# Performance work log

Hardware: AMD Instinct MI355X
Metric: run time of the kernel (lower is better)

## Reference

```python
import jax, jax.numpy as jnp
import numpy as np


def setup_inputs() -> dict:
    key = jax.random.key(0)
    ks = jax.random.split(key, 8)
    B, N, D, H = 8, 512, 64, 64
    user_embeddings = jax.random.normal(ks[0], (B, N, D), dtype=jnp.float32)
    past_lengths = jax.random.randint(ks[1], (B,), 0, N)
    valid_mask = jnp.ones((B, N), dtype=jnp.float32)
    # MLP params: Linear(4D -> H), PReLU (single slope), Linear(H -> 1)
    s1 = 1.0 / np.sqrt(4 * D)
    s2 = 1.0 / np.sqrt(H)
    W1 = jax.random.uniform(ks[2], (H, 4 * D), minval=-s1, maxval=s1, dtype=jnp.float32)
    b1 = jax.random.uniform(ks[3], (H,), minval=-s1, maxval=s1, dtype=jnp.float32)
    prelu_a = jnp.float32(0.25)
    W2 = jax.random.uniform(ks[4], (1, H), minval=-s2, maxval=s2, dtype=jnp.float32)
    b2 = jax.random.uniform(ks[5], (1,), minval=-s2, maxval=s2, dtype=jnp.float32)
    return {"past_lengths": past_lengths, "user_embeddings": user_embeddings,
            "valid_mask": valid_mask, "W1": W1, "b1": b1, "prelu_a": prelu_a,
            "W2": W2, "b2": b2}


def reference(past_lengths, user_embeddings, valid_mask, W1, b1, prelu_a, W2, b2):
    # DIN local activation attention with causal mask.
    # Original math: h = W1 @ concat(Q, K, Q-K, Q*K) + b1 per (q,k) pair.
    # Split W1 into its 4 D-sized blocks so the concat tensor [B,N,N,4D] is
    # never materialized; the pairwise hidden [B,N,N,H] is the only big buffer.
    B, N, D = user_embeddings.shape
    Wq, Wk, Wd, Wm = jnp.split(W1, 4, axis=1)  # each [H, D]
    x = user_embeddings
    # Q and (Q-K)'s +Q part -> per-query term; K and (Q-K)'s -K part -> per-key term
    hq = jnp.einsum('bqd,hd->bqh', x, Wq + Wd)          # [B,N,H]
    hk = jnp.einsum('bkd,hd->bkh', x, Wk - Wd)          # [B,N,H]
    hm = jnp.einsum('bqd,bkd,hd->bqkh', x, x, Wm)       # [B,N,N,H] (Q*K term)
    h = hq[:, :, None, :] + hk[:, None, :, :] + hm + b1
    h = jnp.where(h > 0, h, prelu_a * h)                # PReLU
    scores = jnp.einsum('bqkh,h->bqk', h, W2[0]) + b2[0]  # [B,N,N]
    causal = jnp.tril(jnp.ones((N, N), dtype=scores.dtype))
    scores = scores * causal[None, :, :]
    scores = scores * valid_mask[:, None, :]            # key-side padding mask
    encoded = jnp.einsum('bqk,bkd->bqd', scores, x)     # weighted sum (no softmax)
    return encoded
```

## Files before the change

### kernel.cpp

```cpp
#include <hip/hip_runtime.h>

#define NB 8
#define NN 512

#define WS_WMF 0
#define WS_HQ  4096
#define WS_BF  266240
#define WS_XE  528384

typedef float fx4 __attribute__((ext_vector_type(4)));
typedef short sx8 __attribute__((ext_vector_type(8)));
typedef int   ix4 __attribute__((ext_vector_type(4)));

static __device__ inline unsigned short f2bf(float f) {
    unsigned u = __float_as_uint(f);
    return (unsigned short)((u + 0x7FFFu + ((u >> 16) & 1u)) >> 16);
}

__global__ __launch_bounds__(256) void prep(const float* __restrict__ x,
                                            const float* __restrict__ vm,
                                            const float* __restrict__ W1,
                                            const float* __restrict__ b1,
                                            float* __restrict__ ws) {
    __shared__ float lwq[64 * 65];
    __shared__ float lwk[64 * 65];
    __shared__ float xs[256];
    const int t = threadIdx.x;
    const int blk = blockIdx.x;

    {
        int d = t & 63, hb = t >> 6;
        #pragma unroll 4
        for (int i = 0; i < 16; ++i) {
            int h = i * 4 + hb;
            float a = W1[h * 256 + d];
            float bb = W1[h * 256 + 64 + d];
            float c = W1[h * 256 + 128 + d];
            lwq[d * 65 + h] = a + c;
            lwk[d * 65 + h] = bb - c;
        }
    }
    const int r0 = blk * 4;
    xs[t] = x[r0 * 64 + t];
    __syncthreads();

    {
        int r = t >> 6, h = t & 63;
        const float* xr = xs + r * 64;
        float aq = b1[h], ak = 0.f;
        #pragma unroll
        for (int dd = 0; dd < 64; ++dd) {
            float xv = xr[dd];
            aq = fmaf(xv, lwq[dd * 65 + h], aq);
            ak = fmaf(xv, lwk[dd * 65 + h], ak);
        }
        int row = r0 + r;
        (ws + WS_HQ)[row * 64 + h] = aq;
        unsigned short* bfp = (unsigned short*)(ws + WS_BF);
        int bb = row >> 9, k = row & 511;
        int tt = k >> 4, nn = k & 15;
        int c = 2 + (h >> 5);
        int qd = (h >> 3) & 3, j = h & 7;
        int ln = qd * 16 + nn;
        bfp[((((bb * 32 + tt) * 4 + c) * 64 + ln) << 3) + j] = f2bf(ak);
    }

    if (blk < 256) {
        int b = blk >> 5, t5 = blk & 31;
        if (t < 128) {
            unsigned short* bfp = (unsigned short*)(ws + WS_BF);
            int c = t >> 6, L = t & 63;
            int nn = L & 15, qd = L >> 4;
            const float* src = x + ((b * 512 + t5 * 16 + nn) * 64 + c * 32 + qd * 8);
            fx4 v0 = *(const fx4*)src;
            fx4 v1 = *(const fx4*)(src + 4);
            uint4 o;
            o.x = (unsigned)f2bf(v0[0]) | ((unsigned)f2bf(v0[1]) << 16);
            o.y = (unsigned)f2bf(v0[2]) | ((unsigned)f2bf(v0[3]) << 16);
            o.z = (unsigned)f2bf(v1[0]) | ((unsigned)f2bf(v1[1]) << 16);
            o.w = (unsigned)f2bf(v1[2]) | ((unsigned)f2bf(v1[3]) << 16);
            *(uint4*)(bfp + ((((b * 32 + t5) * 4 + c) * 64 + L) << 3)) = o;
        }
        {
            unsigned short* xep = (unsigned short*)(ws + WS_XE);
            int c32 = t5 >> 1, half = t5 & 1;
            int nt = t >> 6, r = t & 63;
            int L = half * 32 + (r & 31);
            int j0 = (r >> 5) * 4;
            int quad = L >> 4, nn = L & 15;
            unsigned short u[4];
            #pragma unroll
            for (int i = 0; i < 4; ++i) {
                int key = c32 * 32 + quad * 8 + j0 + i;
                float v = x[(b * 512 + key) * 64 + nt * 16 + nn] * vm[b * 512 + key];
                u[i] = f2bf(v);
            }
            uint2 o;
            o.x = (unsigned)u[0] | ((unsigned)u[1] << 16);
            o.y = (unsigned)u[2] | ((unsigned)u[3] << 16);
            *(uint2*)(xep + (((((b * 16 + c32) * 4 + nt) * 64 + L) << 3) + j0)) = o;
        }
    } else if (blk < 258) {
        float* wmf = ws + WS_WMF;
        int e = (blk - 256) * 256 + t;
        int slot = e >> 6, lane = e & 63;
        int ht = slot >> 1, hf = slot & 1;
        int m = lane & 15, qd = lane >> 4;
        int h = ht * 16 + m;
        int dbase = hf * 32 + qd * 8;
        #pragma unroll
        for (int j = 0; j < 8; ++j)
            wmf[e * 8 + j] = W1[h * 256 + 192 + dbase + j];
    }
}

__global__ __launch_bounds__(256, 2) void k2_main(const float* __restrict__ x,
                                                  const float* __restrict__ prelu_a,
                                                  const float* __restrict__ W2,
                                                  const float* __restrict__ b2,
                                                  const float* __restrict__ ws,
                                                  float* __restrict__ out) {
    const int tid  = threadIdx.x;
    const int lane = tid & 63;
    const int w    = tid >> 6;
    const int blk  = blockIdx.x;
    const int b    = blk >> 6;
    const int rest = blk & 63;
    const int m    = rest >> 3;
    const int s    = rest & 7;
    const int n    = lane & 15, quad = lane >> 4;

    const float* wmf = ws + WS_WMF;
    const float* hq  = ws + WS_HQ;
    const unsigned short* bfp = (const unsigned short*)(ws + WS_BF);
    const unsigned short* xep = (const unsigned short*)(ws + WS_XE);

    const float pa  = prelu_a[0];
    const float b2v = b2[0];

    __shared__ uint4 bufS[2][512];
    __shared__ uint4 bufE[2][256];
    __shared__ unsigned strip[4][16];

    float w2r[4][4];
    #pragma unroll
    for (int ht = 0; ht < 4; ++ht) {
        fx4 vw = *(const fx4*)(W2 + ht * 16 + quad * 4);
        #pragma unroll
        for (int r = 0; r < 4; ++r) w2r[ht][r] = vw[r];
    }
    sx8 oh[4];
    #pragma unroll
    for (int ht = 0; ht < 4; ++ht) {
        sx8 a;
        #pragma unroll
        for (int jj = 0; jj < 8; ++jj) {
            int hp = (ht >> 1) * 32 + quad * 8 + jj;
            a[jj] = (hp == ht * 16 + n) ? (short)0x3F80 : (short)0;
        }
        oh[ht] = a;
    }
    const unsigned sel = (quad < 2) ? 0x05040100u : 0x07060302u;

    {
        const uint4* srcS = (const uint4*)(bfp + (unsigned)(b * 32) * 2048);
        bufS[0][tid]       = srcS[tid];
        bufS[0][tid + 256] = srcS[tid + 256];
        bufE[0][tid] = ((const uint4*)(xep + (unsigned)(b * 16) * 2048))[tid];
    }
    __syncthreads();

    int r = 0;
    #pragma unroll 1
    for (int ph = 0; ph < 2; ++ph) {
        const int band = ph ? (15 - m) : m;
        const int q    = band * 32 + s * 4 + w;
        const int bq   = b * 512 + q;
        const int cmax = band;

        float hqr[4][4];
        #pragma unroll
        for (int ht = 0; ht < 4; ++ht) {
            fx4 vh = *(const fx4*)(hq + bq * 64 + ht * 16 + quad * 4);
            #pragma unroll
            for (int rr = 0; rr < 4; ++rr) hqr[ht][rr] = vh[rr];
        }
        float xq[2][8];
        {
            const float* xp = x + bq * 64 + quad * 8;
            fx4 t0 = *(const fx4*)xp;
            fx4 t1 = *(const fx4*)(xp + 4);
            fx4 t2 = *(const fx4*)(xp + 32);
            fx4 t3 = *(const fx4*)(xp + 36);
            #pragma unroll
            for (int jj = 0; jj < 4; ++jj) {
                xq[0][jj] = t0[jj]; xq[0][4 + jj] = t1[jj];
                xq[1][jj] = t2[jj]; xq[1][4 + jj] = t3[jj];
            }
        }
        sx8 afrag[4][2];
        #pragma unroll
        for (int ht = 0; ht < 4; ++ht)
            #pragma unroll
            for (int hf = 0; hf < 2; ++hf) {
                const float* wp = wmf + (((ht * 2 + hf) * 64 + lane) << 3);
                fx4 w0 = *(const fx4*)wp;
                fx4 w1 = *(const fx4*)(wp + 4);
                sx8 a;
                #pragma unroll
                for (int jj = 0; jj < 4; ++jj) {
                    a[jj]     = (short)f2bf(w0[jj] * xq[hf][jj]);
                    a[4 + jj] = (short)f2bf(w1[jj] * xq[hf][4 + jj]);
                }
                afrag[ht][hf] = a;
            }

        fx4 eacc[4];
        #pragma unroll
        for (int nt = 0; nt < 4; ++nt) eacc[nt] = (fx4){0.f, 0.f, 0.f, 0.f};

        for (int c = 0; c <= cmax; ++c, ++r) {
            uint4 st0, st1, stE;
            if (r < 16) {
                int nc = (r + 1 <= m) ? (r + 1) : (r - m);
                const uint4* srcS = (const uint4*)(bfp + (unsigned)(b * 32 + 2 * nc) * 2048);
                st0 = srcS[tid];
                st1 = srcS[tid + 256];
                stE = ((const uint4*)(xep + (unsigned)(b * 16 + nc) * 2048))[tid];
            }

            const unsigned short* ls = (const unsigned short*)&bufS[r & 1][0] + lane * 8;
            sx8 fa0 = *(const sx8*)(ls);
            sx8 fa1 = *(const sx8*)(ls + 512);
            sx8 fa2 = *(const sx8*)(ls + 1024);
            sx8 fa3 = *(const sx8*)(ls + 1536);
            sx8 fb0 = *(const sx8*)(ls + 2048);
            sx8 fb1 = *(const sx8*)(ls + 2560);
            sx8 fb2 = *(const sx8*)(ls + 3072);
            sx8 fb3 = *(const sx8*)(ls + 3584);

            fx4 accA[4], accB[4];
            #pragma unroll
            for (int ht = 0; ht < 4; ++ht) {
                accA[ht] = (fx4){hqr[ht][0], hqr[ht][1], hqr[ht][2], hqr[ht][3]};
                accB[ht] = accA[ht];
            }
            #pragma unroll
            for (int ht = 0; ht < 4; ++ht) {
                accA[ht] = __builtin_amdgcn_mfma_f32_16x16x32_bf16(afrag[ht][0], fa0, accA[ht], 0, 0, 0);
                accB[ht] = __builtin_amdgcn_mfma_f32_16x16x32_bf16(afrag[ht][0], fb0, accB[ht], 0, 0, 0);
            }
            #pragma unroll
            for (int ht = 0; ht < 4; ++ht) {
                accA[ht] = __builtin_amdgcn_mfma_f32_16x16x32_bf16(afrag[ht][1], fa1, accA[ht], 0, 0, 0);
                accB[ht] = __builtin_amdgcn_mfma_f32_16x16x32_bf16(afrag[ht][1], fb1, accB[ht], 0, 0, 0);
            }
            #pragma unroll
            for (int ht = 0; ht < 4; ++ht) {
                accA[ht] = __builtin_amdgcn_mfma_f32_16x16x32_bf16(oh[ht], (ht < 2) ? fa2 : fa3, accA[ht], 0, 0, 0);
                accB[ht] = __builtin_amdgcn_mfma_f32_16x16x32_bf16(oh[ht], (ht < 2) ? fb2 : fb3, accB[ht], 0, 0, 0);
            }

            float s0a = 0.f, s0b = 0.f, s1a = 0.f, s1b = 0.f;
            #pragma unroll
            for (int ht = 0; ht < 2; ++ht)
                #pragma unroll
                for (int rr = 0; rr < 4; ++rr) {
                    float za = accA[ht][rr], zb = accB[ht][rr];
                    s0a = fmaf(w2r[ht][rr], fmaxf(za, za * pa), s0a);
                    s1a = fmaf(w2r[ht][rr], fmaxf(zb, zb * pa), s1a);
                }
            #pragma unroll
            for (int ht = 2; ht < 4; ++ht)
                #pragma unroll
                for (int rr = 0; rr < 4; ++rr) {
                    float za = accA[ht][rr], zb = accB[ht][rr];
                    s0b = fmaf(w2r[ht][rr], fmaxf(za, za * pa), s0b);
                    s1b = fmaf(w2r[ht][rr], fmaxf(zb, zb * pa), s1b);
                }
            float s0 = s0a + s0b, s1 = s1a + s1b;
            s0 += __shfl_xor(s0, 16, 64);
            s0 += __shfl_xor(s0, 32, 64);
            s1 += __shfl_xor(s1, 16, 64);
            s1 += __shfl_xor(s1, 32, 64);
            int k0 = c * 32 + n;
            s0 = (k0 <= q)      ? s0 + b2v : 0.f;
            s1 = (k0 + 16 <= q) ? s1 + b2v : 0.f;

            unsigned packed = (unsigned)f2bf(s0) | ((unsigned)f2bf(s1) << 16);
            if (quad == 0) strip[w][n] = packed;
            const unsigned* sp = &strip[w][(quad & 1) * 8];
            uint4 wv0 = *(const uint4*)sp;
            uint4 wv1 = *(const uint4*)(sp + 4);
            ix4 sw_;
            sw_[0] = (int)__builtin_amdgcn_perm(wv0.y, wv0.x, sel);
            sw_[1] = (int)__builtin_amdgcn_perm(wv0.w, wv0.z, sel);
            sw_[2] = (int)__builtin_amdgcn_perm(wv1.y, wv1.x, sel);
            sw_[3] = (int)__builtin_amdgcn_perm(wv1.w, wv1.z, sel);
            sx8 sfrag = __builtin_bit_cast(sx8, sw_);

            const unsigned short* le = (const unsigned short*)&bufE[r & 1][0] + lane * 8;
            sx8 e0 = *(const sx8*)(le);
            sx8 e1 = *(const sx8*)(le + 512);
            sx8 e2 = *(const sx8*)(le + 1024);
            sx8 e3 = *(const sx8*)(le + 1536);

            eacc[0] = __builtin_amdgcn_mfma_f32_16x16x32_bf16(sfrag, e0, eacc[0], 0, 0, 0);
            eacc[1] = __builtin_amdgcn_mfma_f32_16x16x32_bf16(sfrag, e1, eacc[1], 0, 0, 0);
            eacc[2] = __builtin_amdgcn_mfma_f32_16x16x32_bf16(sfrag, e2, eacc[2], 0, 0, 0);
            eacc[3] = __builtin_amdgcn_mfma_f32_16x16x32_bf16(sfrag, e3, eacc[3], 0, 0, 0);

            if (r < 16) {
                bufS[(r + 1) & 1][tid]       = st0;
                bufS[(r + 1) & 1][tid + 256] = st1;
                bufE[(r + 1) & 1][tid]       = stE;
            }
            __syncthreads();
        }

        float ov = eacc[0][0];
        if (quad == 1) ov = eacc[1][0];
        if (quad == 2) ov = eacc[2][0];
        if (quad == 3) ov = eacc[3][0];
        out[bq * 64 + lane] = ov;
    }
}

extern "C" void kernel_launch(void* const* d_in, const int* in_sizes, int n_in,
                              void* d_out, int out_size, void* d_ws, size_t ws_size,
                              hipStream_t stream) {
    const float* x   = (const float*)d_in[1];
    const float* vmk = (const float*)d_in[2];
    const float* W1  = (const float*)d_in[3];
    const float* b1  = (const float*)d_in[4];
    const float* pa  = (const float*)d_in[5];
    const float* W2  = (const float*)d_in[6];
    const float* b2  = (const float*)d_in[7];
    float* ws  = (float*)d_ws;
    float* out = (float*)d_out;

    hipLaunchKernelGGL(prep, dim3(NB * NN / 4), dim3(256), 0, stream,
                       x, vmk, W1, b1, ws);
    hipLaunchKernelGGL(k2_main, dim3(NB * 64), dim3(256), 0, stream,
                       x, pa, W2, b2, ws, out);
}
```

Before: 103.1 us.

## Process two key chunks per barrier round and vectorize prep matvec

The main kernel now stages two 32-key chunks per double-buffered round, halving the number of __syncthreads barriers and global prefetch rounds across the causal bands. The PReLU/W2 reduction is rewritten with fx4 vector ops. The prep kernel stores the weight tiles transposed with padding so the per-thread dot product can use vector LDS reads. Shared memory per block doubles and more registers are live per round, which may reduce occupancy.

```diff
diff --git a/kernel.cpp b/kernel.cpp
--- a/kernel.cpp
+++ b/kernel.cpp
@@ -22,8 +22,8 @@
                                             const float* __restrict__ W1,
                                             const float* __restrict__ b1,
                                             float* __restrict__ ws) {
-    __shared__ float lwq[64 * 65];
-    __shared__ float lwk[64 * 65];
+    __shared__ float lwq[64 * 68];
+    __shared__ float lwk[64 * 68];
     __shared__ float xs[256];
     const int t = threadIdx.x;
     const int blk = blockIdx.x;
@@ -36,8 +36,8 @@
             float a = W1[h * 256 + d];
             float bb = W1[h * 256 + 64 + d];
             float c = W1[h * 256 + 128 + d];
-            lwq[d * 65 + h] = a + c;
-            lwk[d * 65 + h] = bb - c;
+            lwq[h * 68 + d] = a + c;
+            lwk[h * 68 + d] = bb - c;
         }
     }
     const int r0 = blk * 4;
@@ -46,13 +46,19 @@
 
     {
         int r = t >> 6, h = t & 63;
-        const float* xr = xs + r * 64;
+        const fx4* xr  = (const fx4*)(xs + r * 64);
+        const fx4* wqv = (const fx4*)(lwq + h * 68);
+        const fx4* wkv = (const fx4*)(lwk + h * 68);
         float aq = b1[h], ak = 0.f;
         #pragma unroll
-        for (int dd = 0; dd < 64; ++dd) {
-            float xv = xr[dd];
-            aq = fmaf(xv, lwq[dd * 65 + h], aq);
-            ak = fmaf(xv, lwk[dd * 65 + h], ak);
+        for (int dd = 0; dd < 16; ++dd) {
+            fx4 xv = xr[dd];
+            fx4 wq = wqv[dd];
+            fx4 wk = wkv[dd];
+            aq = fmaf(xv[0], wq[0], aq); aq = fmaf(xv[1], wq[1], aq);
+            aq = fmaf(xv[2], wq[2], aq); aq = fmaf(xv[3], wq[3], aq);
+            ak = fmaf(xv[0], wk[0], ak); ak = fmaf(xv[1], wk[1], ak);
+            ak = fmaf(xv[2], wk[2], ak); ak = fmaf(xv[3], wk[3], ak);
         }
         int row = r0 + r;
         (ws + WS_HQ)[row * 64 + h] = aq;
@@ -105,8 +111,8 @@
         int e = (blk - 256) * 256 + t;
         int slot = e >> 6, lane = e & 63;
         int ht = slot >> 1, hf = slot & 1;
-        int m = lane & 15, qd = lane >> 4;
-        int h = ht * 16 + m;
+        int mm = lane & 15, qd = lane >> 4;
+        int h = ht * 16 + mm;
         int dbase = hf * 32 + qd * 8;
         #pragma unroll
         for (int j = 0; j < 8; ++j)
@@ -129,6 +135,7 @@
     const int m    = rest >> 3;
     const int s    = rest & 7;
     const int n    = lane & 15, quad = lane >> 4;
+    const int RA   = (m + 2) >> 1;
 
     const float* wmf = ws + WS_WMF;
     const float* hq  = ws + WS_HQ;
@@ -138,17 +145,14 @@
     const float pa  = prelu_a[0];
     const float b2v = b2[0];
 
-    __shared__ uint4 bufS[2][512];
-    __shared__ uint4 bufE[2][256];
-    __shared__ unsigned strip[4][16];
-
-    float w2r[4][4];
+    __shared__ uint4 bufS[2][2][512];
+    __shared__ uint4 bufE[2][2][256];
+    __shared__ unsigned strip[4][2][16];
+
+    fx4 w2v[4];
     #pragma unroll
-    for (int ht = 0; ht < 4; ++ht) {
-        fx4 vw = *(const fx4*)(W2 + ht * 16 + quad * 4);
-        #pragma unroll
-        for (int r = 0; r < 4; ++r) w2r[ht][r] = vw[r];
-    }
+    for (int ht = 0; ht < 4; ++ht)
+        w2v[ht] = *(const fx4*)(W2 + ht * 16 + quad * 4);
     sx8 oh[4];
     #pragma unroll
     for (int ht = 0; ht < 4; ++ht) {
@@ -163,28 +167,28 @@
     const unsigned sel = (quad < 2) ? 0x05040100u : 0x07060302u;
 
     {
-        const uint4* srcS = (const uint4*)(bfp + (unsigned)(b * 32) * 2048);
-        bufS[0][tid]       = srcS[tid];
-        bufS[0][tid + 256] = srcS[tid + 256];
-        bufE[0][tid] = ((const uint4*)(xep + (unsigned)(b * 16) * 2048))[tid];
+        int c1i = (m >= 1) ? 1 : 0;
+        const uint4* sS0 = (const uint4*)(bfp + (unsigned)(b * 32) * 2048);
+        const uint4* sS1 = (const uint4*)(bfp + (unsigned)(b * 32 + 2 * c1i) * 2048);
+        bufS[0][0][tid] = sS0[tid]; bufS[0][0][tid + 256] = sS0[tid + 256];
+        bufS[0][1][tid] = sS1[tid]; bufS[0][1][tid + 256] = sS1[tid + 256];
+        bufE[0][0][tid] = ((const uint4*)(xep + (unsigned)(b * 16) * 2048))[tid];
+        bufE[0][1][tid] = ((const uint4*)(xep + (unsigned)(b * 16 + c1i) * 2048))[tid];
     }
     __syncthreads();
 
     int r = 0;
     #pragma unroll 1
     for (int ph = 0; ph < 2; ++ph) {
-        const int band = ph ? (15 - m) : m;
-        const int q    = band * 32 + s * 4 + w;
-        const int bq   = b * 512 + q;
-        const int cmax = band;
-
-        float hqr[4][4];
-        #pragma unroll
-        for (int ht = 0; ht < 4; ++ht) {
-            fx4 vh = *(const fx4*)(hq + bq * 64 + ht * 16 + quad * 4);
-            #pragma unroll
-            for (int rr = 0; rr < 4; ++rr) hqr[ht][rr] = vh[rr];
-        }
+        const int band   = ph ? (15 - m) : m;
+        const int q      = band * 32 + s * 4 + w;
+        const int bq     = b * 512 + q;
+        const int rounds = ph ? (9 - RA) : RA;
+
+        fx4 hqv[4];
+        #pragma unroll
+        for (int ht = 0; ht < 4; ++ht)
+            hqv[ht] = *(const fx4*)(hq + bq * 64 + ht * 16 + quad * 4);
         float xq[2][8];
         {
             const float* xp = x + bq * 64 + quad * 8;
@@ -219,17 +223,8 @@
         #pragma unroll
         for (int nt = 0; nt < 4; ++nt) eacc[nt] = (fx4){0.f, 0.f, 0.f, 0.f};
 
-        for (int c = 0; c <= cmax; ++c, ++r) {
-            uint4 st0, st1, stE;
-            if (r < 16) {
-                int nc = (r + 1 <= m) ? (r + 1) : (r - m);
-                const uint4* srcS = (const uint4*)(bfp + (unsigned)(b * 32 + 2 * nc) * 2048);
-                st0 = srcS[tid];
-                st1 = srcS[tid + 256];
-                stE = ((const uint4*)(xep + (unsigned)(b * 16 + nc) * 2048))[tid];
-            }
-
-            const unsigned short* ls = (const unsigned short*)&bufS[r & 1][0] + lane * 8;
+        auto do_chunk = [&](int c, int sub, int parity) {
+            const unsigned short* ls = (const unsigned short*)&bufS[parity][sub][0] + lane * 8;
             sx8 fa0 = *(const sx8*)(ls);
             sx8 fa1 = *(const sx8*)(ls + 512);
             sx8 fa2 = *(const sx8*)(ls + 1024);
@@ -241,10 +236,7 @@
 
             fx4 accA[4], accB[4];
             #pragma unroll
-            for (int ht = 0; ht < 4; ++ht) {
-                accA[ht] = (fx4){hqr[ht][0], hqr[ht][1], hqr[ht][2], hqr[ht][3]};
-                accB[ht] = accA[ht];
-            }
+            for (int ht = 0; ht < 4; ++ht) { accA[ht] = hqv[ht]; accB[ht] = hqv[ht]; }
             #pragma unroll
             for (int ht = 0; ht < 4; ++ht) {
                 accA[ht] = __builtin_amdgcn_mfma_f32_16x16x32_bf16(afrag[ht][0], fa0, accA[ht], 0, 0, 0);
@@ -261,24 +253,18 @@
                 accB[ht] = __builtin_amdgcn_mfma_f32_16x16x32_bf16(oh[ht], (ht < 2) ? fb2 : fb3, accB[ht], 0, 0, 0);
             }
 
-            float s0a = 0.f, s0b = 0.f, s1a = 0.f, s1b = 0.f;
-            #pragma unroll
-            for (int ht = 0; ht < 2; ++ht)
-                #pragma unroll
-                for (int rr = 0; rr < 4; ++rr) {
-                    float za = accA[ht][rr], zb = accB[ht][rr];
-                    s0a = fmaf(w2r[ht][rr], fmaxf(za, za * pa), s0a);
-                    s1a = fmaf(w2r[ht][rr], fmaxf(zb, zb * pa), s1a);
-                }
-            #pragma unroll
-            for (int ht = 2; ht < 4; ++ht)
-                #pragma unroll
-                for (int rr = 0; rr < 4; ++rr) {
-                    float za = accA[ht][rr], zb = accB[ht][rr];
-                    s0b = fmaf(w2r[ht][rr], fmaxf(za, za * pa), s0b);
-                    s1b = fmaf(w2r[ht][rr], fmaxf(zb, zb * pa), s1b);
-                }
-            float s0 = s0a + s0b, s1 = s1a + s1b;
+            fx4 s0v = (fx4){0.f, 0.f, 0.f, 0.f};
+            fx4 s1v = (fx4){0.f, 0.f, 0.f, 0.f};
+            #pragma unroll
+            for (int ht = 0; ht < 4; ++ht) {
+                fx4 za = accA[ht], zb = accB[ht];
+                fx4 ta = __builtin_elementwise_max(za, za * pa);
+                fx4 tb = __builtin_elementwise_max(zb, zb * pa);
+                s0v = ta * w2v[ht] + s0v;
+                s1v = tb * w2v[ht] + s1v;
+            }
+            float s0 = (s0v[0] + s0v[1]) + (s0v[2] + s0v[3]);
+            float s1 = (s1v[0] + s1v[1]) + (s1v[2] + s1v[3]);
             s0 += __shfl_xor(s0, 16, 64);
             s0 += __shfl_xor(s0, 32, 64);
             s1 += __shfl_xor(s1, 16, 64);
@@ -288,8 +274,8 @@
             s1 = (k0 + 16 <= q) ? s1 + b2v : 0.f;
 
             unsigned packed = (unsigned)f2bf(s0) | ((unsigned)f2bf(s1) << 16);
-            if (quad == 0) strip[w][n] = packed;
-            const unsigned* sp = &strip[w][(quad & 1) * 8];
+            if (quad == 0) strip[w][sub][n] = packed;
+            const unsigned* sp = &strip[w][sub][(quad & 1) * 8];
             uint4 wv0 = *(const uint4*)sp;
             uint4 wv1 = *(const uint4*)(sp + 4);
             ix4 sw_;
@@ -299,7 +285,7 @@
             sw_[3] = (int)__builtin_amdgcn_perm(wv1.w, wv1.z, sel);
             sx8 sfrag = __builtin_bit_cast(sx8, sw_);
 
-            const unsigned short* le = (const unsigned short*)&bufE[r & 1][0] + lane * 8;
+            const unsigned short* le = (const unsigned short*)&bufE[parity][sub][0] + lane * 8;
             sx8 e0 = *(const sx8*)(le);
             sx8 e1 = *(const sx8*)(le + 512);
             sx8 e2 = *(const sx8*)(le + 1024);
@@ -309,11 +295,35 @@
             eacc[1] = __builtin_amdgcn_mfma_f32_16x16x32_bf16(sfrag, e1, eacc[1], 0, 0, 0);
             eacc[2] = __builtin_amdgcn_mfma_f32_16x16x32_bf16(sfrag, e2, eacc[2], 0, 0, 0);
             eacc[3] = __builtin_amdgcn_mfma_f32_16x16x32_bf16(sfrag, e3, eacc[3], 0, 0, 0);
-
-            if (r < 16) {
-                bufS[(r + 1) & 1][tid]       = st0;
-                bufS[(r + 1) & 1][tid + 256] = st1;
-                bufE[(r + 1) & 1][tid]       = stE;
+        };
+
+        #pragma unroll 1
+        for (int i = 0; i < rounds; ++i, ++r) {
+            uint4 st0, st1, st2, st3, stE0, stE1;
+            if (r < 8) {
+                int nr = r + 1, c0n, c1n;
+                if (nr < RA) {
+                    c0n = 2 * nr; c1n = (2 * nr + 1 <= m) ? 2 * nr + 1 : m;
+                } else {
+                    int jj = nr - RA, cb = 15 - m;
+                    c0n = 2 * jj; c1n = (2 * jj + 1 <= cb) ? 2 * jj + 1 : cb;
+                }
+                const uint4* sS0 = (const uint4*)(bfp + (unsigned)(b * 32 + 2 * c0n) * 2048);
+                const uint4* sS1 = (const uint4*)(bfp + (unsigned)(b * 32 + 2 * c1n) * 2048);
+                st0 = sS0[tid]; st1 = sS0[tid + 256];
+                st2 = sS1[tid]; st3 = sS1[tid + 256];
+                stE0 = ((const uint4*)(xep + (unsigned)(b * 16 + c0n) * 2048))[tid];
+                stE1 = ((const uint4*)(xep + (unsigned)(b * 16 + c1n) * 2048))[tid];
+            }
+
+            do_chunk(2 * i, 0, r & 1);
+            if (2 * i + 1 <= band) do_chunk(2 * i + 1, 1, r & 1);
+
+            if (r < 8) {
+                int p2 = (r + 1) & 1;
+                bufS[p2][0][tid] = st0; bufS[p2][0][tid + 256] = st1;
+                bufS[p2][1][tid] = st2; bufS[p2][1][tid + 256] = st3;
+                bufE[p2][0][tid] = stE0; bufE[p2][1][tid] = stE1;
             }
             __syncthreads();
         }
```

Result: no change. 102.6 us (-0.5%).
